# Kernel optimization log

Measured on AMD Instinct MI355X. Metric: run time of the kernel, lower is better.

Reference implementation:

```python
import jax, jax.numpy as jnp
import numpy as np

BIT_SIZE = 8
ES_SIZE = 1
IN_F = 2048
OUT_F = 2048
N = 8192


def posit_quantize(x, nbits, es):
    """Round-to-nearest posit(nbits, es) quantization, returned as float32.

    Posit value: sign * useed^k * 2^e * (1+f), useed = 2^(2^es).
    Regime length rlen = k+2 (k>=0) or -k+1 (k<0); fraction bits =
    nbits - 1(sign) - rlen - es, clamped at 0. Magnitudes are clamped to
    [minpos, maxpos] (posits never round a nonzero value to zero/inf).
    """
    two_es = 2 ** es                      # useed = 2**two_es
    npat = nbits - 2
    maxpos = jnp.float32(2.0 ** (two_es * npat))
    minpos = jnp.float32(2.0 ** (-two_es * npat))

    sign = jnp.sign(x)
    ax = jnp.clip(jnp.abs(x), minpos, maxpos)

    s = jnp.floor(jnp.log2(ax))           # integer power-of-two scale
    k = jnp.floor(s / two_es)             # regime value
    rlen = jnp.where(k >= 0, k + 2.0, -k + 1.0)
    fbits = jnp.maximum(nbits - 1.0 - rlen - es, 0.0)

    m = ax * jnp.exp2(-s)                 # mantissa in [1, 2)
    fscale = jnp.exp2(fbits)
    mq = jnp.round(m * fscale) / fscale   # round fraction to fbits
    # carry: mantissa rounded up to 2.0 -> bump exponent
    s = jnp.where(mq >= 2.0, s + 1.0, s)
    mq = jnp.where(mq >= 2.0, 1.0, mq)

    y = sign * mq * jnp.exp2(s)
    y = jnp.clip(y, -maxpos, maxpos)
    return jnp.where(x == 0, jnp.float32(0.0), y).astype(x.dtype)


def setup_inputs() -> dict:
    key = jax.random.key(0)
    kx, kw, kb = jax.random.split(key, 3)
    x = jax.random.normal(kx, (N, IN_F), dtype=jnp.float32)
    bound = 1.0 / np.sqrt(IN_F)  # nn.Linear default init range
    weight = jax.random.uniform(kw, (OUT_F, IN_F), dtype=jnp.float32,
                                minval=-bound, maxval=bound)
    bias = jax.random.uniform(kb, (OUT_F,), dtype=jnp.float32,
                              minval=-bound, maxval=bound)
    return {"x": x, "weight": weight, "bias": bias}


def reference(x, weight, bias):
    xq = posit_quantize(x, BIT_SIZE, ES_SIZE)
    wq = posit_quantize(weight, BIT_SIZE, ES_SIZE)
    bq = posit_quantize(bias, BIT_SIZE, ES_SIZE)
    # y = xq @ wq^T + bq  (nn.Linear)
    return jnp.einsum('ni,oi->no', xq, wq) + bq
```

## Files before the change

### kernel.cpp

```cpp
#include <hip/hip_runtime.h>

typedef __attribute__((ext_vector_type(8))) short bf16x8;
typedef __attribute__((ext_vector_type(4))) float f32x4;

__device__ __forceinline__ float posit_q(float x) {
  float ax = fabsf(x);
  ax = fmaxf(ax, 0x1p-12f);
  ax = fminf(ax, 0x1p12f);
  int s = (int)(__float_as_uint(ax) >> 23) - 127;
  int k = s >> 1;
  int rlen = (k >= 0) ? (k + 2) : (1 - k);
  int fbits = 6 - rlen;
  fbits = fbits < 0 ? 0 : fbits;
  float m = ax * __uint_as_float((unsigned)(127 - s) << 23);
  float fs = (float)(1 << fbits);
  float inv_fs = __uint_as_float((unsigned)(127 - fbits) << 23);
  float mq = rintf(m * fs) * inv_fs;
  if (mq >= 2.0f) { s += 1; mq = 1.0f; }
  float y = mq * __uint_as_float((unsigned)(127 + s) << 23);
  y = fminf(y, 0x1p12f);
  y = copysignf(y, x);
  return (x == 0.0f) ? 0.0f : y;
}

__device__ __forceinline__ ushort4 quant4_bf16(float4 v) {
  ushort4 o;
  o.x = (ushort)(__float_as_uint(posit_q(v.x)) >> 16);
  o.y = (ushort)(__float_as_uint(posit_q(v.y)) >> 16);
  o.z = (ushort)(__float_as_uint(posit_q(v.z)) >> 16);
  o.w = (ushort)(__float_as_uint(posit_q(v.w)) >> 16);
  return o;
}

__global__ void posit_quant_all(const float* __restrict__ x,
                                const float* __restrict__ w,
                                const float* __restrict__ b,
                                ushort* __restrict__ Xq,
                                ushort* __restrict__ Wq,
                                float* __restrict__ bq,
                                int nx4, int nw4, int nb4) {
  int i = blockIdx.x * blockDim.x + threadIdx.x;
  if (i < nx4) {
    ((ushort4*)Xq)[i] = quant4_bf16(((const float4*)x)[i]);
  } else if (i < nx4 + nw4) {
    int j = i - nx4;
    ((ushort4*)Wq)[j] = quant4_bf16(((const float4*)w)[j]);
  } else if (i < nx4 + nw4 + nb4) {
    int j = i - nx4 - nw4;
    float4 v = ((const float4*)b)[j];
    float4 o;
    o.x = posit_q(v.x); o.y = posit_q(v.y);
    o.z = posit_q(v.z); o.w = posit_q(v.w);
    ((float4*)bq)[j] = o;
  }
}

__device__ __forceinline__ void gl_lds16(const ushort* g, ushort* l) {
  __builtin_amdgcn_global_load_lds(
      (const __attribute__((address_space(1))) void*)g,
      (__attribute__((address_space(3))) void*)l,
      16, 0, 0);
}

__global__ __launch_bounds__(512, 4) void posit_gemm(
    const ushort* __restrict__ A, const ushort* __restrict__ B,
    const float* __restrict__ bq, float* __restrict__ C,
    int M, int N, int K) {
  __shared__ ushort sA[256 * 64];
  __shared__ ushort sB[128 * 64];

  const int tid = threadIdx.x;
  const int wave = tid >> 6;
  const int lane = tid & 63;
  const int wm = wave >> 1;
  const int wn = wave & 1;
  const int m0 = blockIdx.y << 8;
  const int n0 = blockIdx.x << 7;

  const int g8 = lane >> 3;
  const int qe = ((lane & 7) ^ g8) << 3;
  const int rb = (wave << 3) + g8;

  const ushort* Ag = A + (size_t)(m0 + rb) * K + qe;
  const ushort* Bg = B + (size_t)(n0 + rb) * K + qe;
  const size_t rstep = (size_t)64 * K;

  const int wbase = wave << 9;
  ushort* lA0 = sA + wbase;
  ushort* lB0 = sB + wbase;

  const int fr = lane & 15;
  const int t4 = lane >> 4;
  const int pk0 = ((t4 ^ (fr & 7)) << 3);
  const int pk1 = (((4 + t4) ^ (fr & 7)) << 3);

  f32x4 acc[4][4];
#pragma unroll
  for (int i = 0; i < 4; i++)
#pragma unroll
    for (int j = 0; j < 4; j++) acc[i][j] = (f32x4){0.f, 0.f, 0.f, 0.f};

  for (int k0 = 0; k0 < K; k0 += 64) {
#pragma unroll
    for (int r = 0; r < 4; r++)
      gl_lds16(Ag + k0 + r * rstep, lA0 + (r << 12));
#pragma unroll
    for (int r = 0; r < 2; r++)
      gl_lds16(Bg + k0 + r * rstep, lB0 + (r << 12));
    __syncthreads();

#pragma unroll
    for (int kk = 0; kk < 2; kk++) {
      const int pk = kk ? pk1 : pk0;
      bf16x8 fa[4], fb[4];
#pragma unroll
      for (int i = 0; i < 4; i++)
        fa[i] = *(const bf16x8*)(sA + (((wm << 6) + (i << 4) + fr) << 6) + pk);
#pragma unroll
      for (int j = 0; j < 4; j++)
        fb[j] = *(const bf16x8*)(sB + (((wn << 6) + (j << 4) + fr) << 6) + pk);

#pragma unroll
      for (int i = 0; i < 4; i++)
#pragma unroll
        for (int j = 0; j < 4; j++)
          acc[i][j] = __builtin_amdgcn_mfma_f32_16x16x32_bf16(
              fa[i], fb[j], acc[i][j], 0, 0, 0);
    }
    __syncthreads();
  }

  const int row0 = m0 + (wm << 6) + (t4 << 2);
  const int col0 = n0 + (wn << 6) + fr;
#pragma unroll
  for (int j = 0; j < 4; j++) {
    const int col = col0 + (j << 4);
    const float bv = bq[col];
#pragma unroll
    for (int i = 0; i < 4; i++) {
      const int row = row0 + (i << 4);
#pragma unroll
      for (int r = 0; r < 4; r++)
        C[(size_t)(row + r) * N + col] = acc[i][j][r] + bv;
    }
  }
}

extern "C" void kernel_launch(void* const* d_in, const int* in_sizes, int n_in,
                              void* d_out, int out_size, void* d_ws, size_t ws_size,
                              hipStream_t stream) {
  const float* x = (const float*)d_in[0];
  const float* w = (const float*)d_in[1];
  const float* bias = (const float*)d_in[2];
  float* out = (float*)d_out;

  const int out_f = in_sizes[2];
  const int in_f = in_sizes[1] / out_f;
  const int m = in_sizes[0] / in_f;
  const int k = in_f;

  ushort* Xq = (ushort*)d_ws;
  ushort* Wq = Xq + (size_t)m * k;
  float* bquant = (float*)(Wq + (size_t)out_f * k);

  const int nx4 = in_sizes[0] / 4;
  const int nw4 = in_sizes[1] / 4;
  const int nb4 = in_sizes[2] / 4;
  const int total4 = nx4 + nw4 + nb4;
  posit_quant_all<<<(total4 + 255) / 256, 256, 0, stream>>>(
      x, w, bias, Xq, Wq, bquant, nx4, nw4, nb4);

  dim3 grid(out_f / 128, m / 256);
  posit_gemm<<<grid, 512, 0, stream>>>(Xq, Wq, bquant, out, m, out_f, k);
}
```

Before: 184.5 us.

## Enlarge GEMM tile to 256x256 with 4-stage LDS ring prefetch pipeline

Reworks the bf16 MFMA GEMM to use a 256x256 output tile with 8 waves arranged 2x4, each holding 8x4 accumulators. The K step drops to 32, and a four-buffer LDS ring prefetches two K-tiles ahead with explicit vmcnt waits and one barrier per step. The goal is to overlap global-to-LDS loads with MFMA work and to get more reuse from each loaded tile. In exchange it uses more registers and a full 128KB of LDS, and lowers occupancy to 2 blocks per SM.

```diff
diff --git a/kernel.cpp b/kernel.cpp
--- a/kernel.cpp
+++ b/kernel.cpp
@@ -62,82 +62,101 @@
       16, 0, 0);
 }
 
-__global__ __launch_bounds__(512, 4) void posit_gemm(
+#define BAR() do { __builtin_amdgcn_s_barrier(); \
+                   __builtin_amdgcn_sched_barrier(0); } while (0)
+
+__global__ __launch_bounds__(512, 2) void posit_gemm(
     const ushort* __restrict__ A, const ushort* __restrict__ B,
     const float* __restrict__ bq, float* __restrict__ C,
     int M, int N, int K) {
-  __shared__ ushort sA[256 * 64];
-  __shared__ ushort sB[128 * 64];
+  __shared__ ushort lds[65536];
 
   const int tid = threadIdx.x;
   const int wave = tid >> 6;
   const int lane = tid & 63;
-  const int wm = wave >> 1;
-  const int wn = wave & 1;
+  const int wm = wave >> 2;
+  const int wn = wave & 3;
   const int m0 = blockIdx.y << 8;
-  const int n0 = blockIdx.x << 7;
+  const int n0 = blockIdx.x << 8;
 
-  const int g8 = lane >> 3;
-  const int qe = ((lane & 7) ^ g8) << 3;
-  const int rb = (wave << 3) + g8;
+  const int srow = (wave << 4) + (lane >> 2);
+  const int sk = (((lane & 3) ^ (lane >> 4)) << 3);
+  const ushort* Ag = A + (size_t)(m0 + srow) * K + sk;
+  const ushort* Bg = B + (size_t)(n0 + srow) * K + sk;
+  const size_t rstep = (size_t)128 * K;
+  const int sbase = wave << 9;
 
-  const ushort* Ag = A + (size_t)(m0 + rb) * K + qe;
-  const ushort* Bg = B + (size_t)(n0 + rb) * K + qe;
-  const size_t rstep = (size_t)64 * K;
-
-  const int wbase = wave << 9;
-  ushort* lA0 = sA + wbase;
-  ushort* lB0 = sB + wbase;
+#define STAGE(Lb, kt) do {                                         \
+    const ushort* _ag = Ag + ((size_t)(kt) << 5);                  \
+    const ushort* _bg = Bg + ((size_t)(kt) << 5);                  \
+    gl_lds16(_ag,         (Lb) + sbase);                           \
+    gl_lds16(_ag + rstep, (Lb) + 4096 + sbase);                    \
+    gl_lds16(_bg,         (Lb) + 8192 + sbase);                    \
+    gl_lds16(_bg + rstep, (Lb) + 12288 + sbase);                   \
+  } while (0)
 
   const int fr = lane & 15;
   const int t4 = lane >> 4;
-  const int pk0 = ((t4 ^ (fr & 7)) << 3);
-  const int pk1 = (((4 + t4) ^ (fr & 7)) << 3);
+  const int sl = ((t4 ^ (fr >> 2)) << 3);
+  const int arl = (((wm << 7) + fr) << 5) + sl;
+  const int brl = (((wn << 6) + fr) << 5) + sl + 8192;
 
-  f32x4 acc[4][4];
+  f32x4 acc[8][4];
 #pragma unroll
-  for (int i = 0; i < 4; i++)
+  for (int i = 0; i < 8; i++)
 #pragma unroll
     for (int j = 0; j < 4; j++) acc[i][j] = (f32x4){0.f, 0.f, 0.f, 0.f};
 
-  for (int k0 = 0; k0 < K; k0 += 64) {
+#define COMP(Lb) do {                                              \
+    bf16x8 fa[8], fb[4];                                           \
+    _Pragma("unroll")                                              \
+    for (int i = 0; i < 8; i++)                                    \
+      fa[i] = *(const bf16x8*)((Lb) + arl + (i << 9));             \
+    _Pragma("unroll")                                              \
+    for (int j = 0; j < 4; j++)                                    \
+      fb[j] = *(const bf16x8*)((Lb) + brl + (j << 9));             \
+    _Pragma("unroll")                                              \
+    for (int i = 0; i < 8; i++)                                    \
+      _Pragma("unroll")                                            \
+      for (int j = 0; j < 4; j++)                                  \
+        acc[i][j] = __builtin_amdgcn_mfma_f32_16x16x32_bf16(       \
+            fa[i], fb[j], acc[i][j], 0, 0, 0);                     \
+  } while (0)
+
+  const int T = K >> 5;
+
+  STAGE(lds, 0);
+  STAGE(lds + 16384, 1);
+  asm volatile("s_waitcnt vmcnt(4)" ::: "memory");
+  BAR();
+
+#pragma unroll 1
+  for (int it = 0; it < (T >> 2); ++it) {
+    const int t0 = it << 2;
 #pragma unroll
-    for (int r = 0; r < 4; r++)
-      gl_lds16(Ag + k0 + r * rstep, lA0 + (r << 12));
-#pragma unroll
-    for (int r = 0; r < 2; r++)
-      gl_lds16(Bg + k0 + r * rstep, lB0 + (r << 12));
-    __syncthreads();
-
-#pragma unroll
-    for (int kk = 0; kk < 2; kk++) {
-      const int pk = kk ? pk1 : pk0;
-      bf16x8 fa[4], fb[4];
-#pragma unroll
-      for (int i = 0; i < 4; i++)
-        fa[i] = *(const bf16x8*)(sA + (((wm << 6) + (i << 4) + fr) << 6) + pk);
-#pragma unroll
-      for (int j = 0; j < 4; j++)
-        fb[j] = *(const bf16x8*)(sB + (((wn << 6) + (j << 4) + fr) << 6) + pk);
-
-#pragma unroll
-      for (int i = 0; i < 4; i++)
-#pragma unroll
-        for (int j = 0; j < 4; j++)
-          acc[i][j] = __builtin_amdgcn_mfma_f32_16x16x32_bf16(
-              fa[i], fb[j], acc[i][j], 0, 0, 0);
+    for (int u = 0; u < 4; ++u) {
+      const int t = t0 + u;
+      ushort* const cb = lds + (u << 14);
+      ushort* const nb = lds + (((u + 2) & 3) << 14);
+      if (t + 2 < T) {
+        STAGE(nb, t + 2);
+        asm volatile("s_waitcnt vmcnt(4)" ::: "memory");
+      } else {
+        asm volatile("s_waitcnt vmcnt(0)" ::: "memory");
+      }
+      BAR();
+      COMP(cb);
     }
-    __syncthreads();
   }
 
-  const int row0 = m0 + (wm << 6) + (t4 << 2);
+  const int row0 = m0 + (wm << 7) + (t4 << 2);
   const int col0 = n0 + (wn << 6) + fr;
 #pragma unroll
   for (int j = 0; j < 4; j++) {
     const int col = col0 + (j << 4);
     const float bv = bq[col];
 #pragma unroll
-    for (int i = 0; i < 4; i++) {
+    for (int i = 0; i < 8; i++) {
       const int row = row0 + (i << 4);
 #pragma unroll
       for (int r = 0; r < 4; r++)
@@ -170,6 +189,6 @@
   posit_quant_all<<<(total4 + 255) / 256, 256, 0, stream>>>(
       x, w, bias, Xq, Wq, bquant, nx4, nw4, nb4);
 
-  dim3 grid(out_f / 128, m / 256);
+  dim3 grid(out_f / 256, m / 256);
   posit_gemm<<<grid, 512, 0, stream>>>(Xq, Wq, bquant, out, m, out_f, k);
 }
```

After: 189.0 us. 2.5% more time.
